# Performance work log

Hardware: AMD Instinct MI355X
Metric: run time of the kernel (lower is better)

## Reference

```python
import jax, jax.numpy as jnp
import numpy as np

B, S, D, H = 2, 2048, 1024, 16
DK = D // H


def setup_inputs() -> dict:
    key = jax.random.key(0)
    ks = jax.random.split(key, 11)
    s = 1.0 / np.sqrt(D)
    inp = {
        "q": jax.random.normal(ks[0], (B, S, D), jnp.float32),
        "k": jax.random.normal(ks[1], (B, S, D), jnp.float32),
        "v": jax.random.normal(ks[2], (B, S, D), jnp.float32),
        "mask": jnp.tril(jnp.ones((S, S), jnp.int32))[None, None],  # [1,1,S,S] causal
        "wq": jax.random.normal(ks[3], (D, D), jnp.float32) * s,
        "bq": jax.random.normal(ks[4], (D,), jnp.float32) * s,
        "wk": jax.random.normal(ks[5], (D, D), jnp.float32) * s,
        "bk": jax.random.normal(ks[6], (D,), jnp.float32) * s,
        "wv": jax.random.normal(ks[7], (D, D), jnp.float32) * s,
        "bv": jax.random.normal(ks[8], (D,), jnp.float32) * s,
        "wo": jax.random.normal(ks[9], (D, D), jnp.float32) * s,
        "bo": jax.random.normal(ks[10], (D,), jnp.float32) * s,
    }
    return inp


def reference(q, k, v, mask, wq, bq, wk, bk, wv, bv, wo, bo):
    # Linear projections (torch Linear: x @ W.T + b)
    def split_heads(x):  # [B,S,D] -> [B,H,S,DK]
        return x.reshape(B, S, H, DK).transpose(0, 2, 1, 3)

    query = split_heads(q @ wq.T + bq)
    key_ = split_heads(k @ wk.T + bk)
    value = split_heads(v @ wv.T + bv)

    scale = 1.0 / jnp.sqrt(jnp.asarray(DK, q.dtype))
    scores = jnp.einsum("bhqd,bhkd->bhqk", query, key_) * scale
    scores = jnp.where(mask == 0, jnp.asarray(-1e9, scores.dtype), scores)
    attn = jax.nn.softmax(scores, axis=-1)  # dropout=0.0 -> identity
    x = jnp.einsum("bhqk,bhkd->bhqd", attn, value)
    x = x.transpose(0, 2, 1, 3).reshape(B, S, D)
    return x @ wo.T + bo
```

## Files before the change

### kernel.cpp

```cpp
#include <hip/hip_runtime.h>

typedef unsigned short u16;
typedef __bf16 bf16x8 __attribute__((ext_vector_type(8)));
typedef u16 u16x8 __attribute__((ext_vector_type(8)));
typedef float f32x4 __attribute__((ext_vector_type(4)));

constexpr size_t WQo = 12582912;
constexpr size_t WOo = 15728640;
constexpr size_t QPo = 16777216;
constexpr size_t KPo = 20971520;
constexpr size_t VTo = 25165824;
constexpr size_t OOo = 29360128;

#define GLD(g, l) __builtin_amdgcn_global_load_lds( \
    (const __attribute__((address_space(1))) void*)(g), \
    (__attribute__((address_space(3))) void*)(l), 16, 0, 0)

__device__ __forceinline__ u16 f2bf(float f) {
  unsigned u = __builtin_bit_cast(unsigned, f);
  u += 0x7fffu + ((u >> 16) & 1u);
  return (u16)(u >> 16);
}

__device__ __forceinline__ f32x4 zero4() {
  f32x4 z = {0.f, 0.f, 0.f, 0.f};
  return z;
}

__device__ __forceinline__ f32x4 mfma16(u16x8 a, u16x8 b, f32x4 c) {
  return __builtin_amdgcn_mfma_f32_16x16x32_bf16(
      __builtin_bit_cast(bf16x8, a), __builtin_bit_cast(bf16x8, b), c, 0, 0, 0);
}

__global__ __launch_bounds__(256) void cast_all(
    const float4* __restrict__ q, const float4* __restrict__ k, const float4* __restrict__ v,
    const float4* __restrict__ wq, const float4* __restrict__ wk,
    const float4* __restrict__ wv, const float4* __restrict__ wo,
    ushort4* __restrict__ dst)
{
  int i = blockIdx.x * 256 + threadIdx.x;
  constexpr int QN = 1048576;
  constexpr int WN = 262144;
  float4 val;
  if (i < QN)            val = q[i];
  else if (i < 2 * QN)   val = k[i - QN];
  else if (i < 3 * QN)   val = v[i - 2 * QN];
  else {
    int j = i - 3 * QN;
    if (j < WN)          val = wq[j];
    else if (j < 2 * WN) val = wk[j - WN];
    else if (j < 3 * WN) val = wv[j - 2 * WN];
    else                 val = wo[j - 3 * WN];
  }
  ushort4 o;
  o.x = f2bf(val.x); o.y = f2bf(val.y); o.z = f2bf(val.z); o.w = f2bf(val.w);
  dst[i] = o;
}

template <int TM>
__device__ __forceinline__ void gemm_core(
    const u16* __restrict__ A, const u16* __restrict__ W,
    const float* __restrict__ bias, void* __restrict__ outp,
    int m0, int n0, int mode)
{
  constexpr int Kd = 1024;
  constexpr int BM = TM * 32;
  constexpr int AC = BM / 64;
  constexpr int ASZ = BM * 32;
  __shared__ alignas(16) u16 As[2 * ASZ];
  __shared__ alignas(16) u16 Bs[2 * 4096];
  const int tid = threadIdx.x;
  const int wave = tid >> 6, lane = tid & 63;
  const int q4 = lane >> 4, l15 = lane & 15;
  const int wm = (wave >> 1) * (TM * 16), wn = (wave & 1) * 64;

  const u16* asrc[AC]; int adst[AC];
#pragma unroll
  for (int t = 0; t < AC; ++t) {
    const int pos = t * 256 + tid;
    const int lr = pos >> 3, p = pos & 7;
    const int c = p ^ (lr & 7);
    asrc[t] = A + (size_t)(m0 + lr * 2 + (c >> 2)) * Kd + (c & 3) * 8;
    adst[t] = pos * 8;
  }
  const u16* bsrc[2]; int bdst[2];
#pragma unroll
  for (int t = 0; t < 2; ++t) {
    const int pos = t * 256 + tid;
    const int lr = pos >> 3, p = pos & 7;
    const int c = p ^ (lr & 7);
    bsrc[t] = W + (size_t)(n0 + lr * 2 + (c >> 2)) * Kd + (c & 3) * 8;
    bdst[t] = pos * 8;
  }
  int aoff[TM], boff[4];
#pragma unroll
  for (int i = 0; i < TM; ++i) {
    const int m = wm + i * 16 + l15;
    const int lr = m >> 1;
    const int p = ((m & 1) * 4 + q4) ^ (lr & 7);
    aoff[i] = lr * 64 + p * 8;
  }
#pragma unroll
  for (int j = 0; j < 4; ++j) {
    const int m = wn + j * 16 + l15;
    const int lr = m >> 1;
    const int p = ((m & 1) * 4 + q4) ^ (lr & 7);
    boff[j] = lr * 64 + p * 8;
  }

  f32x4 acc[TM][4];
#pragma unroll
  for (int i = 0; i < TM; ++i)
#pragma unroll
    for (int j = 0; j < 4; ++j) acc[i][j] = zero4();

#pragma unroll
  for (int t = 0; t < AC; ++t) GLD(asrc[t], As + adst[t]);
#pragma unroll
  for (int t = 0; t < 2; ++t) GLD(bsrc[t], Bs + bdst[t]);

  for (int it = 0; it < 32; ++it) {
    const int buf = it & 1;
    __syncthreads();
    if (it < 31) {
      const int kt = (it + 1) * 32;
      const int ob = buf ^ 1;
#pragma unroll
      for (int t = 0; t < AC; ++t) GLD(asrc[t] + kt, As + ob * ASZ + adst[t]);
#pragma unroll
      for (int t = 0; t < 2; ++t) GLD(bsrc[t] + kt, Bs + ob * 4096 + bdst[t]);
    }
    const u16* Ab = As + buf * ASZ;
    const u16* Bb = Bs + buf * 4096;
    u16x8 af[TM], bfv[4];
#pragma unroll
    for (int i = 0; i < TM; ++i) af[i] = *(const u16x8*)&Ab[aoff[i]];
#pragma unroll
    for (int j = 0; j < 4; ++j) bfv[j] = *(const u16x8*)&Bb[boff[j]];
#pragma unroll
    for (int i = 0; i < TM; ++i)
#pragma unroll
      for (int j = 0; j < 4; ++j)
        acc[i][j] = mfma16(af[i], bfv[j], acc[i][j]);
  }

#pragma unroll
  for (int i = 0; i < TM; ++i) {
    const int mb = m0 + wm + i * 16 + q4 * 4;
#pragma unroll
    for (int j = 0; j < 4; ++j) {
      const int col = n0 + wn + j * 16 + l15;
      const float bsv = bias[col];
      if (mode == 1) {
        const int bb = mb >> 11, s = mb & 2047, hh = col >> 6, dk = col & 63;
        ushort4 pk;
        pk.x = f2bf(acc[i][j][0] + bsv);
        pk.y = f2bf(acc[i][j][1] + bsv);
        pk.z = f2bf(acc[i][j][2] + bsv);
        pk.w = f2bf(acc[i][j][3] + bsv);
        *(ushort4*)&((u16*)outp)[((size_t)(bb * 16 + hh) * 64 + dk) * 2048 + s] = pk;
      } else {
#pragma unroll
        for (int r = 0; r < 4; ++r) {
          const float val = acc[i][j][r] + bsv;
          const int m = mb + r;
          if (mode == 0) {
            const int bb = m >> 11, s = m & 2047, hh = col >> 6, dk = col & 63;
            ((u16*)outp)[((size_t)(bb * 16 + hh) * 2048 + s) * 64 + dk] = f2bf(val);
          } else {
            ((float*)outp)[(size_t)m * 1024 + col] = val;
          }
        }
      }
    }
  }
}

__global__ __launch_bounds__(256) void proj_gemm(
    u16* __restrict__ ws, const float* __restrict__ bq,
    const float* __restrict__ bk, const float* __restrict__ bv)
{
  const int id = blockIdx.x;
  const int z = id >> 8, rem = id & 255;
  const int bx = rem >> 5, by = rem & 31;
  const u16* A = ws + (size_t)z * 4194304;
  const u16* W = ws + WQo + (size_t)z * 1048576;
  const float* bias = (z == 0) ? bq : ((z == 1) ? bk : bv);
  u16* outp = ws + QPo + (size_t)z * 4194304;
  gemm_core<4>(A, W, bias, outp, by * 128, bx * 128, (z == 2) ? 1 : 0);
}

__global__ __launch_bounds__(256) void out_gemm(
    const u16* __restrict__ ws, const float* __restrict__ bo, float* __restrict__ out)
{
  const int id = blockIdx.x;
  const int bx = id >> 6, by = id & 63;
  gemm_core<2>(ws + OOo, ws + WOo, bo, out, by * 64, bx * 128, 3);
}

__global__ __launch_bounds__(256) void flash_attn(u16* __restrict__ ws)
{
  constexpr int S = 2048;
  const int a = blockIdx.x;
  const int b = 31 - blockIdx.x;
  const int bh = blockIdx.y;
  const int bb = bh >> 4, h = bh & 15;
  const int tid = threadIdx.x;
  const int wave = tid >> 6, lane = tid & 63;
  const int q4 = lane >> 4, l15 = lane & 15;

  __shared__ u16 QsA[64 * 64];
  __shared__ u16 QsB[64 * 64];
  __shared__ u16 Ks[2][64 * 64];
  __shared__ u16 Vs[2][64 * 64];

  const u16* Qg = ws + QPo + (size_t)bh * S * 64;
  const u16* Kg = ws + KPo + (size_t)bh * S * 64;
  const u16* Vg = ws + VTo + (size_t)bh * 64 * S;
  u16* Og = ws + OOo;

  const int ch0 = wave * 128 + lane;
  const int ch1 = ch0 + 64;
  const int r0 = ch0 >> 3, c0 = (ch0 & 7) ^ (r0 & 7);
  const int r1 = ch1 >> 3, c1 = (ch1 & 7) ^ (r1 & 7);

  GLD(Qg + (size_t)(a * 64 + r0) * 64 + c0 * 8, QsA + wave * 1024);
  GLD(Qg + (size_t)(a * 64 + r1) * 64 + c1 * 8, QsA + wave * 1024 + 512);
  GLD(Qg + (size_t)(b * 64 + r0) * 64 + c0 * 8, QsB + wave * 1024);
  GLD(Qg + (size_t)(b * 64 + r1) * 64 + c1 * 8, QsB + wave * 1024 + 512);
  GLD(Kg + (size_t)r0 * 64 + c0 * 8, Ks[0] + wave * 1024);
  GLD(Kg + (size_t)r1 * 64 + c1 * 8, Ks[0] + wave * 1024 + 512);
  GLD(Vg + (size_t)r0 * S + c0 * 8, Vs[0] + wave * 1024);
  GLD(Vg + (size_t)r1 * S + c1 * 8, Vs[0] + wave * 1024 + 512);
  __syncthreads();

  u16x8 qfA[2], qfB[2];
  {
    const int row = wave * 16 + l15;
#pragma unroll
    for (int kk = 0; kk < 2; ++kk) {
      const int c = (kk * 4 + q4) ^ (row & 7);
      qfA[kk] = *(const u16x8*)&QsA[row * 64 + c * 8];
      qfB[kk] = *(const u16x8*)&QsB[row * 64 + c * 8];
    }
  }
  u16* Ps = QsA + wave * 1024;

  f32x4 oA[4], oB[4];
  float lA[4], lB[4];
#pragma unroll
  for (int j = 0; j < 4; ++j) { oA[j] = zero4(); oB[j] = zero4(); }
#pragma unroll
  for (int r = 0; r < 4; ++r) { lA[r] = 0.f; lB[r] = 0.f; }

  for (int kt = 0; kt <= b; ++kt) {
    const u16* Ksb = Ks[kt & 1];
    const u16* Vsb = Vs[kt & 1];
    if (kt < b) {
      const u16* Kt = Kg + (size_t)(kt + 1) * 64 * 64;
      u16* Kd = Ks[(kt + 1) & 1];
      u16* Vd = Vs[(kt + 1) & 1];
      GLD(Kt + (size_t)r0 * 64 + c0 * 8, Kd + wave * 1024);
      GLD(Kt + (size_t)r1 * 64 + c1 * 8, Kd + wave * 1024 + 512);
      GLD(Vg + (size_t)r0 * S + (kt + 1) * 64 + c0 * 8, Vd + wave * 1024);
      GLD(Vg + (size_t)r1 * S + (kt + 1) * 64 + c1 * 8, Vd + wave * 1024 + 512);
    }

    auto process = [&](const u16x8* qf, f32x4* o_acc, float* l_p, int qt, bool diag) {
      f32x4 sf[4];
#pragma unroll
      for (int j = 0; j < 4; ++j) {
        f32x4 z = zero4();
        const int row = j * 16 + l15;
#pragma unroll
        for (int kk = 0; kk < 2; ++kk) {
          const int c = (kk * 4 + q4) ^ (row & 7);
          z = mfma16(qf[kk], *(const u16x8*)&Ksb[row * 64 + c * 8], z);
        }
        sf[j] = z;
      }
      if (diag) {
        const int rowg0 = qt * 64 + wave * 16 + q4 * 4;
#pragma unroll
        for (int j = 0; j < 4; ++j) {
          const int colg = kt * 64 + j * 16 + l15;
#pragma unroll
          for (int r = 0; r < 4; ++r) {
            float val = sf[j][r] * 0.125f;
            if (colg > rowg0 + r) val = -__builtin_inff();
            sf[j][r] = __expf(val);
          }
        }
      } else {
#pragma unroll
        for (int j = 0; j < 4; ++j)
#pragma unroll
          for (int r = 0; r < 4; ++r)
            sf[j][r] = __expf(sf[j][r] * 0.125f);
      }
#pragma unroll
      for (int j = 0; j < 4; ++j)
#pragma unroll
        for (int r = 0; r < 4; ++r) l_p[r] += sf[j][r];

#pragma unroll
      for (int j = 0; j < 4; ++j)
#pragma unroll
        for (int r = 0; r < 4; ++r) {
          const int m = q4 * 4 + r;
          const int srow = j * 16 + l15;
          const int pos = m * 64 + (((srow >> 3) ^ (m & 7)) << 3) + (srow & 7);
          Ps[pos] = f2bf(sf[j][r]);
        }
      u16x8 pf[2];
#pragma unroll
      for (int kk = 0; kk < 2; ++kk) {
        const int c = (kk * 4 + q4) ^ (l15 & 7);
        pf[kk] = *(const u16x8*)&Ps[l15 * 64 + c * 8];
      }
#pragma unroll
      for (int j = 0; j < 4; ++j) {
        const int row = j * 16 + l15;
#pragma unroll
        for (int kk = 0; kk < 2; ++kk) {
          const int c = (kk * 4 + q4) ^ (row & 7);
          o_acc[j] = mfma16(pf[kk], *(const u16x8*)&Vsb[row * 64 + c * 8], o_acc[j]);
        }
      }
    };

    process(qfB, oB, lB, b, kt == b);
    if (kt <= a) process(qfA, oA, lA, a, kt == a);
    __syncthreads();
  }

#pragma unroll
  for (int off = 1; off < 16; off <<= 1)
#pragma unroll
    for (int r = 0; r < 4; ++r) {
      lA[r] += __shfl_xor(lA[r], off, 64);
      lB[r] += __shfl_xor(lB[r], off, 64);
    }

#pragma unroll
  for (int r = 0; r < 4; ++r) {
    const float invA = 1.f / lA[r];
    const float invB = 1.f / lB[r];
    const int sA = a * 64 + wave * 16 + q4 * 4 + r;
    const int sB = b * 64 + wave * 16 + q4 * 4 + r;
    const size_t baseA = ((size_t)(bb * 2048 + sA)) * 1024 + h * 64;
    const size_t baseB = ((size_t)(bb * 2048 + sB)) * 1024 + h * 64;
#pragma unroll
    for (int j = 0; j < 4; ++j) {
      Og[baseA + j * 16 + l15] = f2bf(oA[j][r] * invA);
      Og[baseB + j * 16 + l15] = f2bf(oB[j][r] * invB);
    }
  }
}

extern "C" void kernel_launch(void* const* d_in, const int* in_sizes, int n_in,
                              void* d_out, int out_size, void* d_ws, size_t ws_size,
                              hipStream_t stream)
{
  const float* q  = (const float*)d_in[0];
  const float* k  = (const float*)d_in[1];
  const float* v  = (const float*)d_in[2];
  const float* wq = (const float*)d_in[4];
  const float* bq = (const float*)d_in[5];
  const float* wk = (const float*)d_in[6];
  const float* bk = (const float*)d_in[7];
  const float* wv = (const float*)d_in[8];
  const float* bv = (const float*)d_in[9];
  const float* wo = (const float*)d_in[10];
  const float* bo = (const float*)d_in[11];
  u16* ws = (u16*)d_ws;
  float* out = (float*)d_out;

  cast_all<<<16384, 256, 0, stream>>>(
      (const float4*)q, (const float4*)k, (const float4*)v,
      (const float4*)wq, (const float4*)wk, (const float4*)wv, (const float4*)wo,
      (ushort4*)ws);
  proj_gemm<<<768, 256, 0, stream>>>(ws, bq, bk, bv);
  flash_attn<<<dim3(16, 32), 256, 0, stream>>>(ws);
  out_gemm<<<512, 256, 0, stream>>>(ws, bo, out);
}
```

Baseline: 230.3 us.

## Fuse fp32-to-bf16 activation cast into projection GEMM A-tile loads

The projection GEMM now reads fp32 q/k/v directly and converts them to bf16 in registers before storing into swizzled LDS. This removes the separate cast pass over the activations and its write and re-read of a bf16 copy, leaving a small weights-only cast kernel. The A-tile prefetch is now register-staged, with the LDS write placed after the MFMA loop, instead of using async global-to-LDS loads, which adds register pressure and VALU conversion work. The output GEMM also changes from 64-row to 128-row tiles, halving its grid to 256 blocks.

```diff
diff --git a/kernel.cpp b/kernel.cpp
--- a/kernel.cpp
+++ b/kernel.cpp
@@ -32,40 +32,40 @@
       __builtin_bit_cast(bf16x8, a), __builtin_bit_cast(bf16x8, b), c, 0, 0, 0);
 }
 
-__global__ __launch_bounds__(256) void cast_all(
-    const float4* __restrict__ q, const float4* __restrict__ k, const float4* __restrict__ v,
+__device__ __forceinline__ u16x8 cvt8(f32x4 lo, f32x4 hi) {
+  u16x8 r;
+  r[0] = f2bf(lo[0]); r[1] = f2bf(lo[1]); r[2] = f2bf(lo[2]); r[3] = f2bf(lo[3]);
+  r[4] = f2bf(hi[0]); r[5] = f2bf(hi[1]); r[6] = f2bf(hi[2]); r[7] = f2bf(hi[3]);
+  return r;
+}
+
+__global__ __launch_bounds__(256) void cast_w(
     const float4* __restrict__ wq, const float4* __restrict__ wk,
     const float4* __restrict__ wv, const float4* __restrict__ wo,
     ushort4* __restrict__ dst)
 {
   int i = blockIdx.x * 256 + threadIdx.x;
-  constexpr int QN = 1048576;
   constexpr int WN = 262144;
   float4 val;
-  if (i < QN)            val = q[i];
-  else if (i < 2 * QN)   val = k[i - QN];
-  else if (i < 3 * QN)   val = v[i - 2 * QN];
-  else {
-    int j = i - 3 * QN;
-    if (j < WN)          val = wq[j];
-    else if (j < 2 * WN) val = wk[j - WN];
-    else if (j < 3 * WN) val = wv[j - 2 * WN];
-    else                 val = wo[j - 3 * WN];
-  }
+  if (i < WN)          val = wq[i];
+  else if (i < 2 * WN) val = wk[i - WN];
+  else if (i < 3 * WN) val = wv[i - 2 * WN];
+  else                 val = wo[i - 3 * WN];
   ushort4 o;
   o.x = f2bf(val.x); o.y = f2bf(val.y); o.z = f2bf(val.z); o.w = f2bf(val.w);
   dst[i] = o;
 }
 
-template <int TM>
+template <int TM, bool AFUSE>
 __device__ __forceinline__ void gemm_core(
-    const u16* __restrict__ A, const u16* __restrict__ W,
+    const void* __restrict__ Ap, const u16* __restrict__ W,
     const float* __restrict__ bias, void* __restrict__ outp,
     int m0, int n0, int mode)
 {
   constexpr int Kd = 1024;
   constexpr int BM = TM * 32;
   constexpr int AC = BM / 64;
+  constexpr int ACH = BM / 64;
   constexpr int ASZ = BM * 32;
   __shared__ alignas(16) u16 As[2 * ASZ];
   __shared__ alignas(16) u16 Bs[2 * 4096];
@@ -74,14 +74,27 @@
   const int q4 = lane >> 4, l15 = lane & 15;
   const int wm = (wave >> 1) * (TM * 16), wn = (wave & 1) * 64;
 
-  const u16* asrc[AC]; int adst[AC];
-#pragma unroll
-  for (int t = 0; t < AC; ++t) {
-    const int pos = t * 256 + tid;
-    const int lr = pos >> 3, p = pos & 7;
-    const int c = p ^ (lr & 7);
-    asrc[t] = A + (size_t)(m0 + lr * 2 + (c >> 2)) * Kd + (c & 3) * 8;
-    adst[t] = pos * 8;
+  const float* afsrc[AFUSE ? ACH : 1]; int afdst[AFUSE ? ACH : 1];
+  const u16*   asrc [AFUSE ? 1 : AC]; int adst [AFUSE ? 1 : AC];
+  if (AFUSE) {
+#pragma unroll
+    for (int u = 0; u < ACH; ++u) {
+      const int ci = u * 256 + tid;
+      const int m = ci >> 2, k4 = ci & 3;
+      const int lr = m >> 1;
+      const int p = ((m & 1) * 4 + k4) ^ (lr & 7);
+      afsrc[u] = (const float*)Ap + (size_t)(m0 + m) * Kd + k4 * 8;
+      afdst[u] = lr * 64 + p * 8;
+    }
+  } else {
+#pragma unroll
+    for (int t = 0; t < AC; ++t) {
+      const int pos = t * 256 + tid;
+      const int lr = pos >> 3, p = pos & 7;
+      const int c = p ^ (lr & 7);
+      asrc[t] = (const u16*)Ap + (size_t)(m0 + lr * 2 + (c >> 2)) * Kd + (c & 3) * 8;
+      adst[t] = pos * 8;
+    }
   }
   const u16* bsrc[2]; int bdst[2];
 #pragma unroll
@@ -114,19 +127,37 @@
 #pragma unroll
     for (int j = 0; j < 4; ++j) acc[i][j] = zero4();
 
-#pragma unroll
-  for (int t = 0; t < AC; ++t) GLD(asrc[t], As + adst[t]);
+  if (AFUSE) {
+#pragma unroll
+    for (int u = 0; u < ACH; ++u) {
+      f32x4 lo = *(const f32x4*)(afsrc[u]);
+      f32x4 hi = *(const f32x4*)(afsrc[u] + 4);
+      *(u16x8*)&As[afdst[u]] = cvt8(lo, hi);
+    }
+  } else {
+#pragma unroll
+    for (int t = 0; t < AC; ++t) GLD(asrc[t], As + adst[t]);
+  }
 #pragma unroll
   for (int t = 0; t < 2; ++t) GLD(bsrc[t], Bs + bdst[t]);
 
   for (int it = 0; it < 32; ++it) {
     const int buf = it & 1;
     __syncthreads();
+    const int kt = (it + 1) * 32;
+    const int ob = buf ^ 1;
+    f32x4 lo[AFUSE ? ACH : 1], hi[AFUSE ? ACH : 1];
     if (it < 31) {
-      const int kt = (it + 1) * 32;
-      const int ob = buf ^ 1;
-#pragma unroll
-      for (int t = 0; t < AC; ++t) GLD(asrc[t] + kt, As + ob * ASZ + adst[t]);
+      if (AFUSE) {
+#pragma unroll
+        for (int u = 0; u < ACH; ++u) {
+          lo[u] = *(const f32x4*)(afsrc[u] + kt);
+          hi[u] = *(const f32x4*)(afsrc[u] + kt + 4);
+        }
+      } else {
+#pragma unroll
+        for (int t = 0; t < AC; ++t) GLD(asrc[t] + kt, As + ob * ASZ + adst[t]);
+      }
 #pragma unroll
       for (int t = 0; t < 2; ++t) GLD(bsrc[t] + kt, Bs + ob * 4096 + bdst[t]);
     }
@@ -142,6 +173,11 @@
 #pragma unroll
       for (int j = 0; j < 4; ++j)
         acc[i][j] = mfma16(af[i], bfv[j], acc[i][j]);
+    if (AFUSE && it < 31) {
+#pragma unroll
+      for (int u = 0; u < ACH; ++u)
+        *(u16x8*)&As[ob * ASZ + afdst[u]] = cvt8(lo[u], hi[u]);
+    }
   }
 
 #pragma unroll
@@ -177,25 +213,27 @@
 }
 
 __global__ __launch_bounds__(256) void proj_gemm(
-    u16* __restrict__ ws, const float* __restrict__ bq,
-    const float* __restrict__ bk, const float* __restrict__ bv)
+    const float* __restrict__ q, const float* __restrict__ k,
+    const float* __restrict__ v, u16* __restrict__ ws,
+    const float* __restrict__ bq, const float* __restrict__ bk,
+    const float* __restrict__ bv)
 {
   const int id = blockIdx.x;
   const int z = id >> 8, rem = id & 255;
   const int bx = rem >> 5, by = rem & 31;
-  const u16* A = ws + (size_t)z * 4194304;
+  const float* A = (z == 0) ? q : ((z == 1) ? k : v);
   const u16* W = ws + WQo + (size_t)z * 1048576;
   const float* bias = (z == 0) ? bq : ((z == 1) ? bk : bv);
   u16* outp = ws + QPo + (size_t)z * 4194304;
-  gemm_core<4>(A, W, bias, outp, by * 128, bx * 128, (z == 2) ? 1 : 0);
+  gemm_core<4, true>(A, W, bias, outp, by * 128, bx * 128, (z == 2) ? 1 : 0);
 }
 
 __global__ __launch_bounds__(256) void out_gemm(
     const u16* __restrict__ ws, const float* __restrict__ bo, float* __restrict__ out)
 {
   const int id = blockIdx.x;
-  const int bx = id >> 6, by = id & 63;
-  gemm_core<2>(ws + OOo, ws + WOo, bo, out, by * 64, bx * 128, 3);
+  const int bx = id >> 5, by = id & 31;
+  gemm_core<4, false>(ws + OOo, ws + WOo, bo, out, by * 128, bx * 128, 3);
 }
 
 __global__ __launch_bounds__(256) void flash_attn(u16* __restrict__ ws)
@@ -376,11 +414,10 @@
   u16* ws = (u16*)d_ws;
   float* out = (float*)d_out;
 
-  cast_all<<<16384, 256, 0, stream>>>(
-      (const float4*)q, (const float4*)k, (const float4*)v,
+  cast_w<<<4096, 256, 0, stream>>>(
       (const float4*)wq, (const float4*)wk, (const float4*)wv, (const float4*)wo,
-      (ushort4*)ws);
-  proj_gemm<<<768, 256, 0, stream>>>(ws, bq, bk, bv);
+      (ushort4*)(ws + WQo));
+  proj_gemm<<<768, 256, 0, stream>>>(q, k, v, ws, bq, bk, bv);
   flash_attn<<<dim3(16, 32), 256, 0, stream>>>(ws);
-  out_gemm<<<512, 256, 0, stream>>>(ws, bo, out);
-}
+  out_gemm<<<256, 256, 0, stream>>>(ws, bo, out);
+}
```

Measured after the change: 243.5 us. 1.06x slower.
